# Performance work log

Hardware: AMD Instinct MI355X
Metric: run time of the kernel (lower is better)

## Reference

```python
import jax, jax.numpy as jnp
import numpy as np

ALPHA = 1.0
BETA = 6.0
GAMMA = 1.0
N_DATA = 50000
IS_MSS = True
LOG2PI = float(np.log(2.0 * np.pi))


def _log_density_gaussian(x, mu, logvar):
    # elementwise Gaussian log-density
    return -0.5 * (LOG2PI + logvar) - 0.5 * (x - mu) ** 2 * jnp.exp(-logvar)


def _log_importance_weight_matrix(batch_size, n_data):
    # Faithful to the reference torch implementation (incl. the column-1 and
    # [M-1,0] stratified-weight overwrites done via flat strided assignment).
    N = float(n_data)
    M = float(batch_size - 1)
    strat = (N - M) / (N * M)
    W = jnp.full((batch_size, batch_size), 1.0 / M, dtype=jnp.float32)
    idx = jnp.arange(batch_size)
    W = W.at[idx, idx].set(1.0 / N)
    W = W.at[:, 1].set(strat)
    W = W.at[batch_size - 2, 0].set(strat)
    return jnp.log(W)


def setup_inputs() -> dict:
    key = jax.random.key(0)
    k1, k2, k3, k4, k5 = jax.random.split(key, 5)
    B, D = 1024, 64
    return {
        "recon_x": jax.random.normal(k1, (B, 3, 64, 64), dtype=jnp.float32),
        "x": jax.random.normal(k2, (B, 3, 64, 64), dtype=jnp.float32),
        "mu": jax.random.normal(k3, (B, D), dtype=jnp.float32),
        "logvar": jax.random.normal(k4, (B, D), dtype=jnp.float32),
        "noise": jax.random.normal(k5, (B, D), dtype=jnp.float32),
    }


def reference(recon_x, x, mu, logvar, noise):
    B, D = mu.shape
    # reconstruction: MSE with sum reduction
    reconstruction_loss = jnp.sum((recon_x - x) ** 2)

    # reparameterized latent sample (noise supplied deterministically)
    z = mu + noise * jnp.exp(0.5 * logvar)

    # log q(z|x) and log p(z), each summed over latent dims -> [B]
    log_q_zCx = _log_density_gaussian(z, mu, logvar).sum(axis=1)
    log_pz = _log_density_gaussian(z, jnp.zeros_like(z), jnp.zeros_like(z)).sum(axis=1)

    # pairwise matrix log q(z_i | x_j): [B, B, D]
    mat_log_qz = _log_density_gaussian(z[:, None, :], mu[None, :, :], logvar[None, :, :])
    if IS_MSS:
        log_iw = _log_importance_weight_matrix(B, N_DATA)
        mat_log_qz = mat_log_qz + log_iw[:, :, None]

    log_qz = jax.scipy.special.logsumexp(mat_log_qz.sum(axis=2), axis=1)  # [B]
    log_prod_qzi = jax.scipy.special.logsumexp(mat_log_qz, axis=1).sum(axis=1)  # [B]

    mi_loss = jnp.mean(log_q_zCx - log_qz)
    tc_loss = jnp.mean(log_qz - log_prod_qzi)
    dw_kl_loss = jnp.mean(log_prod_qzi - log_pz)

    return reconstruction_loss + (ALPHA * mi_loss + BETA * tc_loss + GAMMA * dw_kl_loss)
```

## Files before the change

### kernel.cpp

```cpp
#include <hip/hip_runtime.h>
#include <math.h>

typedef __attribute__((ext_vector_type(8))) short short8;
typedef __attribute__((ext_vector_type(4))) float f32x4;

#define BB 1024
#define DD 64
#define NPIX (1024*3*64*64)

#define LN2PI_F  1.8378770664093453f
#define LOG2E_F  1.4426950408889634f

#define INV_M  (1.0f/1023.0f)
#define INV_N  (1.0f/50000.0f)
#define STRATF ((float)((50000.0-1023.0)/(50000.0*1023.0)))
#define NEGBIG (-3.0e38f)

#define L2_INVM  (-9.9985904f)
#define L2_INVN  (-15.6096405f)
#define L2_STRAT (-10.0284195f)

#define WS_RP    0
#define WS_LQC   2048
#define WS_LPZ   3072
#define WS_LQZ   4096
#define WS_LPR   5120
#define WS_Z     6144
#define WS_Z2    71680
#define WS_A     137216
#define WS_B     202752
#define WS_C     268288
#define WS_KC    333824
#define WS_QZP   334848
#define WS_SEDP  400384
#define WS_ABF   924672
#define WS_BBF   990208

__device__ __forceinline__ float fexp2(float x){ return __builtin_amdgcn_exp2f(x); }
__device__ __forceinline__ float flog2(float x){ return __builtin_amdgcn_logf(x); }
__device__ __forceinline__ unsigned short tobf(float f){
    unsigned int u = __float_as_uint(f);
    u = (u + 0x7FFFu + ((u >> 16) & 1u)) >> 16;
    return (unsigned short)u;
}

__global__ __launch_bounds__(256) void k_recon_prep(const float4* __restrict__ rx,
                                                    const float4* __restrict__ x,
                                                    const float* __restrict__ mu,
                                                    const float* __restrict__ logvar,
                                                    const float* __restrict__ noise,
                                                    float* __restrict__ ws) {
    int bid = blockIdx.x, t = threadIdx.x;
    if (bid < 2048) {
        int gid = bid * 256 + t;
        const int n4 = NPIX / 4, stride = 2048 * 256;
        float acc = 0.f;
        for (int idx = gid; idx < n4; idx += stride) {
            float4 a = rx[idx], b = x[idx];
            float d0 = a.x - b.x, d1 = a.y - b.y, d2 = a.z - b.z, d3 = a.w - b.w;
            acc = fmaf(d0, d0, acc); acc = fmaf(d1, d1, acc);
            acc = fmaf(d2, d2, acc); acc = fmaf(d3, d3, acc);
        }
        __shared__ float red[256];
        red[t] = acc; __syncthreads();
        for (int o = 128; o > 0; o >>= 1) {
            if (t < o) red[t] += red[t + o];
            __syncthreads();
        }
        if (t == 0) ws[WS_RP + bid] = red[0];
    } else {
        int pb = bid - 2048;
        int d = t & 63, w = t >> 6;
        int i = pb * 4 + w;
        int idx = i * 64 + d;
        float m = mu[idx], lvv = logvar[idx], n = noise[idx];
        float sh   = fexp2(0.5f * LOG2E_F * lvv);
        float z    = fmaf(n, sh, m);
        float eneg = fexp2(-LOG2E_F * lvv);
        float a = -0.5f * LOG2E_F * eneg;
        float b = -2.0f * a * m;
        float c = fmaf(a, m * m, -0.5f * LOG2E_F * (LN2PI_F + lvv));
        float z2 = z * z;
        ws[WS_Z  + idx] = z;  ws[WS_Z2 + idx] = z2;
        ws[WS_A  + idx] = a;  ws[WS_B  + idx] = b;  ws[WS_C + idx] = c;
        unsigned short* abf = (unsigned short*)(ws + WS_ABF);
        unsigned short* bbf = (unsigned short*)(ws + WS_BBF);
        abf[i * 128 + d]      = tobf(z2);
        abf[i * 128 + 64 + d] = tobf(z);
        bbf[i * 128 + d]      = tobf(a);
        bbf[i * 128 + 64 + d] = tobf(b);
        float lqc = -0.5f * (LN2PI_F + lvv + n * n);
        float lpz = -0.5f * (LN2PI_F + z2);
        float kc  = c;
        for (int off = 32; off > 0; off >>= 1) {
            lqc += __shfl_xor(lqc, off, 64);
            lpz += __shfl_xor(lpz, off, 64);
            kc  += __shfl_xor(kc,  off, 64);
        }
        if (d == 0) { ws[WS_LQC + i] = lqc; ws[WS_LPZ + i] = lpz; ws[WS_KC + i] = kc; }
    }
}

__global__ __launch_bounds__(256) void k_pair(float* __restrict__ ws) {
    __shared__ char smem[32768];
    int bid = blockIdx.x, t = threadIdx.x;
    int lane = t & 63, w = t >> 6;
    if (bid < 256) {
        unsigned short* As = (unsigned short*)smem;
        unsigned short* Bs = As + 64 * 128;
        const unsigned short* abf = (const unsigned short*)(ws + WS_ABF);
        const unsigned short* bbf = (const unsigned short*)(ws + WS_BBF);
        int i0 = (bid & 15) * 64, j0 = (bid >> 4) * 64;
        for (int e = 0; e < 4; e++) {
            int lin = e * 256 + t, row = lin >> 4, cu = lin & 15, su = cu ^ (row & 7);
            *(float4*)&As[row * 128 + su * 8] = *(const float4*)&abf[(i0 + row) * 128 + cu * 8];
            *(float4*)&Bs[row * 128 + su * 8] = *(const float4*)&bbf[(j0 + row) * 128 + cu * 8];
        }
        __syncthreads();
        int lo = lane & 15, g = lane >> 4;
        int wi = (w >> 1) * 32, wj = (w & 1) * 32;
        f32x4 acc[2][2] = {};
        for (int kk = 0; kk < 4; kk++) {
            short8 af[2], bfr[2];
            #pragma unroll
            for (int fy = 0; fy < 2; fy++) {
                int rA = wi + fy * 16 + lo;
                int cA = (kk * 4 + g) ^ (rA & 7);
                af[fy] = *(const short8*)&As[rA * 128 + cA * 8];
            }
            #pragma unroll
            for (int fx = 0; fx < 2; fx++) {
                int rB = wj + fx * 16 + lo;
                int cB = (kk * 4 + g) ^ (rB & 7);
                bfr[fx] = *(const short8*)&Bs[rB * 128 + cB * 8];
            }
            #pragma unroll
            for (int fy = 0; fy < 2; fy++)
                #pragma unroll
                for (int fx = 0; fx < 2; fx++)
                    acc[fy][fx] = __builtin_amdgcn_mfma_f32_16x16x32_bf16(af[fy], bfr[fx], acc[fy][fx], 0, 0, 0);
        }
        int jA = j0 + wj + lo;
        float kcv0 = ws[WS_KC + jA], kcv1 = ws[WS_KC + jA + 16];
        int pc = (j0 >> 5) + (w & 1);
        #pragma unroll
        for (int fy = 0; fy < 2; fy++) {
            #pragma unroll
            for (int r = 0; r < 4; r++) {
                int i = i0 + wi + fy * 16 + g * 4 + r;
                float vv0, vv1;
                {
                    int j = jA;
                    float lw = (j == 1) ? L2_STRAT : (i == j) ? L2_INVN
                             : (i == 1022 && j == 0) ? L2_STRAT : L2_INVM;
                    vv0 = acc[fy][0][r] + kcv0 + 64.0f * lw;
                }
                {
                    int j = jA + 16;
                    float lw = (j == 1) ? L2_STRAT : (i == j) ? L2_INVN
                             : (i == 1022 && j == 0) ? L2_STRAT : L2_INVM;
                    vv1 = acc[fy][1][r] + kcv1 + 64.0f * lw;
                }
                float m = fmaxf(vv0, vv1);
                float s = fexp2(vv0 - m) + fexp2(vv1 - m);
                for (int off = 1; off < 16; off <<= 1) {
                    float om = __shfl_xor(m, off, 64);
                    float os = __shfl_xor(s, off, 64);
                    float M = fmaxf(m, om);
                    s = s * fexp2(m - M) + os * fexp2(om - M);
                    m = M;
                }
                if (lo == 0) {
                    ws[WS_QZP + ((pc << 10) + i) * 2]     = m;
                    ws[WS_QZP + ((pc << 10) + i) * 2 + 1] = s;
                }
            }
        }
    } else {
        float* sacc = (float*)smem;
        int sid = bid - 256;
        int ic = sid & 127, jc = sid >> 7;
        int i0 = ic * 8, d = lane;
        int jbase = jc * 128 + w * 32;
        float z2r[8], zr[8], se[8];
        #pragma unroll
        for (int k = 0; k < 8; k++) {
            z2r[k] = ws[WS_Z2 + (i0 + k) * 64 + d];
            zr[k]  = ws[WS_Z  + (i0 + k) * 64 + d];
            se[k] = 0.f;
        }
        #pragma unroll 2
        for (int jj = 0; jj < 32; jj++) {
            int gidx = (jbase + jj) * 64 + d;
            float av = ws[WS_A + gidx], bv = ws[WS_B + gidx], cv = ws[WS_C + gidx];
            #pragma unroll
            for (int k = 0; k < 8; k++) {
                float u = fmaf(av, z2r[k], fmaf(bv, zr[k], cv));
                se[k] += fexp2(u);
            }
        }
        #pragma unroll
        for (int k = 0; k < 8; k++) sacc[w * 512 + k * 64 + d] = se[k];
        __syncthreads();
        int k0 = w * 2;
        for (int k = k0; k < k0 + 2; k++) {
            float tot = sacc[k * 64 + d] + sacc[512 + k * 64 + d]
                      + sacc[1024 + k * 64 + d] + sacc[1536 + k * 64 + d];
            ws[WS_SEDP + ((jc << 10) + i0 + k) * 64 + d] = tot;
        }
    }
}

__global__ __launch_bounds__(256) void k_post(float* __restrict__ ws) {
    int t = threadIdx.x, lane = t & 63, w = t >> 6;
    int i = blockIdx.x * 4 + w;
    float m = NEGBIG, s = 0.f;
    if (lane < 32) {
        m = ws[WS_QZP + ((lane << 10) + i) * 2];
        s = ws[WS_QZP + ((lane << 10) + i) * 2 + 1];
    }
    for (int off = 1; off < 64; off <<= 1) {
        float om = __shfl_xor(m, off, 64);
        float os = __shfl_xor(s, off, 64);
        float M = fmaxf(m, om);
        s = s * fexp2(m - M) + os * fexp2(om - M);
        m = M;
    }
    if (lane == 0) ws[WS_LQZ + i] = (m + flog2(s)) * (1.0f / LOG2E_F);
    int d = lane;
    float se = 0.f;
    for (int c = 0; c < 8; c++) se += ws[WS_SEDP + ((c << 10) + i) * 64 + d];
    float z2 = ws[WS_Z2 + i * 64 + d], z = ws[WS_Z + i * 64 + d];
    auto E = [&](int j) -> float {
        int gidx = j * 64 + d;
        return fexp2(fmaf(ws[WS_A + gidx], z2, fmaf(ws[WS_B + gidx], z, ws[WS_C + gidx])));
    };
    float sid = INV_M * se;
    if (i != 1)    sid += (INV_N  - INV_M) * E(i);
    sid += (STRATF - INV_M) * E(1);
    if (i == 1022) sid += (STRATF - INV_M) * E(0);
    float lg = flog2(sid);
    for (int off = 1; off < 64; off <<= 1) lg += __shfl_xor(lg, off, 64);
    if (d == 0) ws[WS_LPR + i] = lg * (1.0f / LOG2E_F);
}

__global__ __launch_bounds__(256) void k_final(const float* __restrict__ ws,
                                               float* __restrict__ out) {
    int t = threadIdx.x;
    float a0 = 0, a1 = 0, a2 = 0, a3 = 0, a4 = 0;
    for (int idx = t; idx < 2048; idx += 256) a0 += ws[WS_RP + idx];
    for (int idx = t; idx < BB; idx += 256) {
        a1 += ws[WS_LQC + idx];
        a2 += ws[WS_LPZ + idx];
        a3 += ws[WS_LQZ + idx];
        a4 += ws[WS_LPR + idx];
    }
    __shared__ float red[256];
    float vals[5] = {a0, a1, a2, a3, a4};
    float res[5];
    for (int q = 0; q < 5; q++) {
        red[t] = vals[q]; __syncthreads();
        for (int o = 128; o > 0; o >>= 1) {
            if (t < o) red[t] += red[t + o];
            __syncthreads();
        }
        res[q] = red[0]; __syncthreads();
    }
    if (t == 0) {
        float recon = res[0], slqc = res[1], slpz = res[2], slqz = res[3], slpr = res[4];
        out[0] = recon + (slqc + 5.f * (slqz - slpr) - slpz) * (1.0f / (float)BB);
    }
}

extern "C" void kernel_launch(void* const* d_in, const int* in_sizes, int n_in,
                              void* d_out, int out_size, void* d_ws, size_t ws_size,
                              hipStream_t stream) {
    (void)in_sizes; (void)n_in; (void)out_size; (void)ws_size;
    const float* rx = (const float*)d_in[0];
    const float* x  = (const float*)d_in[1];
    const float* mu = (const float*)d_in[2];
    const float* lv = (const float*)d_in[3];
    const float* nz = (const float*)d_in[4];
    float* ws  = (float*)d_ws;
    float* out = (float*)d_out;

    k_recon_prep<<<2304, 256, 0, stream>>>((const float4*)rx, (const float4*)x, mu, lv, nz, ws);
    k_pair      <<<1280, 256, 0, stream>>>(ws);
    k_post      <<<256,  256, 0, stream>>>(ws);
    k_final     <<<1,    256, 0, stream>>>(ws, out);
}
```

Measured before the change: 47.44 us.

## Overlap recon reduction with pairwise work and fold final reduce into post

Moves the small latent-prep work into its own kernel and runs the large MSE reduction concurrently with the pairwise MFMA and exp-sum blocks in a single fused launch. The recon loop is fully unrolled with a fixed rep count over fewer blocks. The final scalar reduction is merged into k_post using an atomic last-block counter, removing one launch. This trades launch overhead and serialization for a global atomic and threadfence.

Measured after the change: 65.49 us. 1.38x slower.

```diff
diff --git a/kernel.cpp b/kernel.cpp
--- a/kernel.cpp
+++ b/kernel.cpp
@@ -35,6 +35,12 @@
 #define WS_SEDP  400384
 #define WS_ABF   924672
 #define WS_BBF   990208
+#define WS_CNT   1055744
+
+#define NB_RECON 1536
+#define NB_MM    256
+#define NB_SED   1024
+#define RECON_REPS 8
 
 __device__ __forceinline__ float fexp2(float x){ return __builtin_amdgcn_exp2f(x); }
 __device__ __forceinline__ float flog2(float x){ return __builtin_amdgcn_logf(x); }
@@ -44,73 +50,73 @@
     return (unsigned short)u;
 }
 
-__global__ __launch_bounds__(256) void k_recon_prep(const float4* __restrict__ rx,
-                                                    const float4* __restrict__ x,
-                                                    const float* __restrict__ mu,
-                                                    const float* __restrict__ logvar,
-                                                    const float* __restrict__ noise,
-                                                    float* __restrict__ ws) {
+__global__ __launch_bounds__(256) void k_prep(const float* __restrict__ mu,
+                                              const float* __restrict__ logvar,
+                                              const float* __restrict__ noise,
+                                              float* __restrict__ ws) {
+    int t = threadIdx.x, d = t & 63, w = t >> 6;
+    int i = blockIdx.x * 4 + w;
+    int idx = i * 64 + d;
+    if (blockIdx.x == 0 && t == 0) *((int*)(ws + WS_CNT)) = 0;
+    float m = mu[idx], lvv = logvar[idx], n = noise[idx];
+    float sh   = fexp2(0.5f * LOG2E_F * lvv);
+    float z    = fmaf(n, sh, m);
+    float eneg = fexp2(-LOG2E_F * lvv);
+    float a = -0.5f * LOG2E_F * eneg;
+    float b = -2.0f * a * m;
+    float c = fmaf(a, m * m, -0.5f * LOG2E_F * (LN2PI_F + lvv));
+    float z2 = z * z;
+    ws[WS_Z  + idx] = z;  ws[WS_Z2 + idx] = z2;
+    ws[WS_A  + idx] = a;  ws[WS_B  + idx] = b;  ws[WS_C + idx] = c;
+    unsigned short* abf = (unsigned short*)(ws + WS_ABF);
+    unsigned short* bbf = (unsigned short*)(ws + WS_BBF);
+    abf[i * 128 + d]      = tobf(z2);
+    abf[i * 128 + 64 + d] = tobf(z);
+    bbf[i * 128 + d]      = tobf(a);
+    bbf[i * 128 + 64 + d] = tobf(b);
+    float lqc = -0.5f * (LN2PI_F + lvv + n * n);
+    float lpz = -0.5f * (LN2PI_F + z2);
+    float kc  = c;
+    for (int off = 32; off > 0; off >>= 1) {
+        lqc += __shfl_xor(lqc, off, 64);
+        lpz += __shfl_xor(lpz, off, 64);
+        kc  += __shfl_xor(kc,  off, 64);
+    }
+    if (d == 0) { ws[WS_LQC + i] = lqc; ws[WS_LPZ + i] = lpz; ws[WS_KC + i] = kc; }
+}
+
+__global__ __launch_bounds__(256) void k_fused(const float4* __restrict__ rx,
+                                               const float4* __restrict__ x,
+                                               float* __restrict__ ws) {
+    __shared__ char smem[32768];
     int bid = blockIdx.x, t = threadIdx.x;
-    if (bid < 2048) {
+    int lane = t & 63, w = t >> 6;
+    if (bid < NB_RECON) {
         int gid = bid * 256 + t;
-        const int n4 = NPIX / 4, stride = 2048 * 256;
+        const int stride = NB_RECON * 256;
         float acc = 0.f;
-        for (int idx = gid; idx < n4; idx += stride) {
+        #pragma unroll
+        for (int rep = 0; rep < RECON_REPS; rep++) {
+            int idx = gid + rep * stride;
             float4 a = rx[idx], b = x[idx];
             float d0 = a.x - b.x, d1 = a.y - b.y, d2 = a.z - b.z, d3 = a.w - b.w;
             acc = fmaf(d0, d0, acc); acc = fmaf(d1, d1, acc);
             acc = fmaf(d2, d2, acc); acc = fmaf(d3, d3, acc);
         }
-        __shared__ float red[256];
+        float* red = (float*)smem;
         red[t] = acc; __syncthreads();
         for (int o = 128; o > 0; o >>= 1) {
             if (t < o) red[t] += red[t + o];
             __syncthreads();
         }
         if (t == 0) ws[WS_RP + bid] = red[0];
-    } else {
-        int pb = bid - 2048;
-        int d = t & 63, w = t >> 6;
-        int i = pb * 4 + w;
-        int idx = i * 64 + d;
-        float m = mu[idx], lvv = logvar[idx], n = noise[idx];
-        float sh   = fexp2(0.5f * LOG2E_F * lvv);
-        float z    = fmaf(n, sh, m);
-        float eneg = fexp2(-LOG2E_F * lvv);
-        float a = -0.5f * LOG2E_F * eneg;
-        float b = -2.0f * a * m;
-        float c = fmaf(a, m * m, -0.5f * LOG2E_F * (LN2PI_F + lvv));
-        float z2 = z * z;
-        ws[WS_Z  + idx] = z;  ws[WS_Z2 + idx] = z2;
-        ws[WS_A  + idx] = a;  ws[WS_B  + idx] = b;  ws[WS_C + idx] = c;
-        unsigned short* abf = (unsigned short*)(ws + WS_ABF);
-        unsigned short* bbf = (unsigned short*)(ws + WS_BBF);
-        abf[i * 128 + d]      = tobf(z2);
-        abf[i * 128 + 64 + d] = tobf(z);
-        bbf[i * 128 + d]      = tobf(a);
-        bbf[i * 128 + 64 + d] = tobf(b);
-        float lqc = -0.5f * (LN2PI_F + lvv + n * n);
-        float lpz = -0.5f * (LN2PI_F + z2);
-        float kc  = c;
-        for (int off = 32; off > 0; off >>= 1) {
-            lqc += __shfl_xor(lqc, off, 64);
-            lpz += __shfl_xor(lpz, off, 64);
-            kc  += __shfl_xor(kc,  off, 64);
-        }
-        if (d == 0) { ws[WS_LQC + i] = lqc; ws[WS_LPZ + i] = lpz; ws[WS_KC + i] = kc; }
-    }
-}
-
-__global__ __launch_bounds__(256) void k_pair(float* __restrict__ ws) {
-    __shared__ char smem[32768];
-    int bid = blockIdx.x, t = threadIdx.x;
-    int lane = t & 63, w = t >> 6;
-    if (bid < 256) {
+    } else if (bid < NB_RECON + NB_MM) {
+        int mmid = bid - NB_RECON;
         unsigned short* As = (unsigned short*)smem;
         unsigned short* Bs = As + 64 * 128;
         const unsigned short* abf = (const unsigned short*)(ws + WS_ABF);
         const unsigned short* bbf = (const unsigned short*)(ws + WS_BBF);
-        int i0 = (bid & 15) * 64, j0 = (bid >> 4) * 64;
+        int i0 = (mmid & 15) * 64, j0 = (mmid >> 4) * 64;
         for (int e = 0; e < 4; e++) {
             int lin = e * 256 + t, row = lin >> 4, cu = lin & 15, su = cu ^ (row & 7);
             *(float4*)&As[row * 128 + su * 8] = *(const float4*)&abf[(i0 + row) * 128 + cu * 8];
@@ -178,7 +184,7 @@
         }
     } else {
         float* sacc = (float*)smem;
-        int sid = bid - 256;
+        int sid = bid - NB_RECON - NB_MM;
         int ic = sid & 127, jc = sid >> 7;
         int i0 = ic * 8, d = lane;
         int jbase = jc * 128 + w * 32;
@@ -211,7 +217,8 @@
     }
 }
 
-__global__ __launch_bounds__(256) void k_post(float* __restrict__ ws) {
+__global__ __launch_bounds__(256) void k_post(float* __restrict__ ws,
+                                              float* __restrict__ out) {
     int t = threadIdx.x, lane = t & 63, w = t >> 6;
     int i = blockIdx.x * 4 + w;
     float m = NEGBIG, s = 0.f;
@@ -242,13 +249,19 @@
     float lg = flog2(sid);
     for (int off = 1; off < 64; off <<= 1) lg += __shfl_xor(lg, off, 64);
     if (d == 0) ws[WS_LPR + i] = lg * (1.0f / LOG2E_F);
-}
-
-__global__ __launch_bounds__(256) void k_final(const float* __restrict__ ws,
-                                               float* __restrict__ out) {
-    int t = threadIdx.x;
+
+    __shared__ bool isLast;
+    __syncthreads();
+    __threadfence();
+    if (t == 0) {
+        int v = atomicAdd((int*)(ws + WS_CNT), 1);
+        isLast = (v == (int)gridDim.x - 1);
+    }
+    __syncthreads();
+    if (!isLast) return;
+    __threadfence();
     float a0 = 0, a1 = 0, a2 = 0, a3 = 0, a4 = 0;
-    for (int idx = t; idx < 2048; idx += 256) a0 += ws[WS_RP + idx];
+    for (int idx = t; idx < NB_RECON; idx += 256) a0 += ws[WS_RP + idx];
     for (int idx = t; idx < BB; idx += 256) {
         a1 += ws[WS_LQC + idx];
         a2 += ws[WS_LPZ + idx];
@@ -284,8 +297,7 @@
     float* ws  = (float*)d_ws;
     float* out = (float*)d_out;
 
-    k_recon_prep<<<2304, 256, 0, stream>>>((const float4*)rx, (const float4*)x, mu, lv, nz, ws);
-    k_pair      <<<1280, 256, 0, stream>>>(ws);
-    k_post      <<<256,  256, 0, stream>>>(ws);
-    k_final     <<<1,    256, 0, stream>>>(ws, out);
-}
+    k_prep <<<256, 256, 0, stream>>>(mu, lv, nz, ws);
+    k_fused<<<NB_RECON + NB_MM + NB_SED, 256, 0, stream>>>((const float4*)rx, (const float4*)x, ws);
+    k_post <<<256, 256, 0, stream>>>(ws, out);
+}
```
